# Optimization experiments

Measured on AMD Instinct MI355X. Metric: run time of the kernel, lower is better.

## Reference

```python
import jax, jax.numpy as jnp
import numpy as np

NEG_INF = jnp.float32(-1e30)
HASH_PRIME = jnp.int32(1000003)
BLANK_INDEX = 0
BEAM_WIDTH = 32
TOP_PATHS = 1


def _beam_search_single(logp, length):
    """CTC prefix beam search for one utterance.
    logp: [T, C] log-probabilities. length: scalar int32.
    Returns (neg_log_prob [P], lengths [P], labels [P, T]).
    """
    T, C = logp.shape
    W = BEAM_WIDTH
    classes = jnp.arange(C, dtype=jnp.int32)
    tpos = jnp.arange(T, dtype=jnp.int32)
    N = W + W * C  # stay candidates + extend candidates

    seqs0 = jnp.zeros((W, T), jnp.int32)
    lens0 = jnp.zeros((W,), jnp.int32)
    hashes0 = jnp.arange(W, dtype=jnp.int32)  # distinct -> no spurious merging
    pb0 = jnp.full((W,), NEG_INF, jnp.float32).at[0].set(0.0)  # empty prefix, ends-in-blank
    pnb0 = jnp.full((W,), NEG_INF, jnp.float32)

    def step(state, inp):
        seqs, lens, hashes, pb, pnb = state
        lp, t = inp  # lp: [C]
        last = jnp.where(lens > 0, seqs[jnp.arange(W), jnp.maximum(lens - 1, 0)], -1)
        lp_last = jnp.where(last >= 0, lp[jnp.maximum(last, 0)], NEG_INF)
        ptot = jnp.logaddexp(pb, pnb)
        # --- stay candidates (same prefix): blank emission + repeated last label
        stay_pb = ptot + lp[BLANK_INDEX]
        stay_pnb = pnb + lp_last
        # --- extend candidates (W, C): prefix + c, c != blank
        ext_pnb = jnp.where(classes[None, :] == last[:, None],
                            pb[:, None] + lp[None, :],      # repeat label needs blank gap
                            ptot[:, None] + lp[None, :])
        ext_pnb = jnp.where(classes[None, :] == BLANK_INDEX, NEG_INF, ext_pnb)
        ext_pb = jnp.full((W, C), NEG_INF, jnp.float32)
        ext_hash = hashes[:, None] * HASH_PRIME + (classes[None, :] + 1)
        cand_pb = jnp.concatenate([stay_pb, ext_pb.reshape(-1)])
        cand_pnb = jnp.concatenate([stay_pnb, ext_pnb.reshape(-1)])
        cand_hash = jnp.concatenate([hashes, ext_hash.reshape(-1)])
        # --- merge candidates sharing the same prefix (by rolling hash)
        order = jnp.argsort(cand_hash)
        h_s = cand_hash[order]
        pb_s, pnb_s = cand_pb[order], cand_pnb[order]
        new_seg = jnp.concatenate([jnp.ones((1,), jnp.int32),
                                   (h_s[1:] != h_s[:-1]).astype(jnp.int32)])
        seg_id = jnp.cumsum(new_seg) - 1

        def seg_lse(x):
            m = jax.ops.segment_max(x, seg_id, num_segments=N)
            s = jax.ops.segment_sum(jnp.exp(x - m[seg_id]), seg_id, num_segments=N)
            return m + jnp.log(s)

        pb_m = seg_lse(pb_s)[seg_id]
        pnb_m = seg_lse(pnb_s)[seg_id]
        first = new_seg == 1
        pb_s = jnp.where(first, pb_m, NEG_INF)
        pnb_s = jnp.where(first, pnb_m, NEG_INF)
        tot = jnp.logaddexp(pb_s, pnb_s)
        # --- beam pruning
        _, top_idx = jax.lax.top_k(tot, W)
        sel = order[top_idx]  # indices into flat candidate list
        is_ext = sel >= W
        parent = jnp.where(is_ext, (sel - W) // C, sel)
        cls = jnp.where(is_ext, (sel - W) % C, 0).astype(jnp.int32)
        new_pb = pb_s[top_idx]
        new_pnb = pnb_s[top_idx]
        new_hash = cand_hash[sel]
        p_seqs = seqs[parent]
        p_lens = lens[parent]
        new_seqs = jnp.where(is_ext[:, None] & (tpos[None, :] == p_lens[:, None]),
                             cls[:, None], p_seqs)
        new_lens = p_lens + is_ext.astype(jnp.int32)
        # only advance while t < data_length
        active = t < length
        seqs = jnp.where(active, new_seqs, seqs)
        lens = jnp.where(active, new_lens, lens)
        hashes = jnp.where(active, new_hash, hashes)
        pb = jnp.where(active, new_pb, pb)
        pnb = jnp.where(active, new_pnb, pnb)
        return (seqs, lens, hashes, pb, pnb), None

    (seqs, lens, hashes, pb, pnb), _ = jax.lax.scan(
        step, (seqs0, lens0, hashes0, pb0, pnb0), (logp, tpos))
    tot = jnp.logaddexp(pb, pnb)
    top_tot, top_i = jax.lax.top_k(tot, TOP_PATHS)
    return -top_tot, lens[top_i], seqs[top_i]


def setup_inputs() -> dict:
    key = jax.random.key(0)
    k1, k2 = jax.random.split(key)
    data = jax.random.normal(k1, (512, 64, 128), jnp.float32)
    data = jax.nn.log_softmax(data, axis=-1)  # layer expects log probs (from_logits=False)
    data_length = jax.random.randint(k2, (64,), 1, 513, dtype=jnp.int32)
    return {"data": data, "data_length": data_length}


def reference(data, data_length):
    # data: [max_time, batch, num_classes] log probs -> [batch, T, C]
    logp = jnp.transpose(data, (1, 0, 2))
    probs, lengths, predicted = jax.vmap(_beam_search_single)(logp, data_length)
    # top_paths == 1 path of _select_most_likely_path: plain reshape
    B = predicted.shape[0]
    T = predicted.shape[2]
    best = predicted.reshape(B, T)
    lens = lengths.reshape(B)
    # _mask_out_junk_values: fill positions >= length with blank_index
    mask = jnp.arange(T, dtype=lens.dtype)[None, :] < lens[:, None]
    return jnp.where(mask, best, jnp.int32(BLANK_INDEX))
```

## Files before the change

kernel.cpp:

```cpp
#include <hip/hip_runtime.h>
#include <stdint.h>

#define T_MAX 512
#define BATCH 64
#define NCLS  128
#define BEAM  32
#define TBL   6144
#define NEGF  (-1e30f)
#define EMPTYK ((int)0x80000000)
#define HPRIME 1000003u
#define SCAP  256

__device__ __forceinline__ float lae(float a, float b) {
  float mx = fmaxf(a, b);
  return mx + log1pf(expf(-fabsf(a - b)));
}
__device__ __forceinline__ unsigned encf(float x) {
  unsigned v = __float_as_uint(x);
  return (v & 0x80000000u) ? ~v : (v | 0x80000000u);
}
__device__ __forceinline__ float decf(unsigned u) {
  unsigned v = (u & 0x80000000u) ? (u ^ 0x80000000u) : ~u;
  return __uint_as_float(v);
}
__device__ __forceinline__ unsigned lowkey(unsigned h) {
  return 0xFFFFFFFFu - (h ^ 0x80000000u);
}

__device__ __forceinline__ int tbl_insert(int* key, int h) {
  unsigned x = (unsigned)h * 2654435761u;
  x ^= x >> 16;
  int j = (int)(((unsigned long long)x * (unsigned long long)TBL) >> 32);
  for (;;) {
    int cur = key[j];
    if (cur == EMPTYK) cur = atomicCAS(&key[j], EMPTYK, h);
    if (cur == EMPTYK || cur == h) return j;
    ++j; if (j == TBL) j = 0;
  }
}

__device__ __forceinline__ unsigned long long shflx64(unsigned long long v, int m) {
  unsigned lo = (unsigned)__shfl_xor((int)(unsigned)v, m, 64);
  unsigned hi = (unsigned)__shfl_xor((int)(unsigned)(v >> 32), m, 64);
  return ((unsigned long long)hi << 32) | lo;
}

__device__ __forceinline__ unsigned bitonic64_u32_desc(int ln, unsigned v) {
  #pragma unroll
  for (int size = 2; size <= 64; size <<= 1) {
    #pragma unroll
    for (int stride = size >> 1; stride > 0; stride >>= 1) {
      const unsigned o = (unsigned)__shfl_xor((int)v, stride, 64);
      const bool keepMax = (((ln & size) == 0) == ((ln & stride) == 0));
      v = keepMax ? (v > o ? v : o) : (v < o ? v : o);
    }
  }
  return v;
}

__global__ __launch_bounds__(512, 1)
void ctc_beam_kernel(const float* __restrict__ data,
                     const int* __restrict__ dlen,
                     int* __restrict__ out) {
  __shared__ int       tkey[TBL];
  __shared__ unsigned  tmax[TBL];
  __shared__ unsigned  tsum[TBL];
  __shared__ unsigned  tmin[TBL];
  __shared__ unsigned short bp[T_MAX * BEAM];
  __shared__ __align__(16) float lpbuf[2][NCLS];
  __shared__ int   bhash[2][BEAM];
  __shared__ float bpb[2][BEAM], bpnb[2][BEAM];
  __shared__ int   blen[2][BEAM], blast[2][BEAM];
  __shared__ float sptot[BEAM], s_pb[BEAM], s_pnb[BEAM], s_pnbm[BEAM];
  __shared__ int   stay_slot[BEAM];
  __shared__ unsigned char mergeTo[BEAM * NCLS];
  __shared__ int mergeCnt[BEAM], mergeFrom[BEAM];
  __shared__ unsigned thsub[64];
  __shared__ int anom, ovf;
  __shared__ int scnt[2];
  __shared__ unsigned long long skey[SCAP + 16];
  __shared__ unsigned sidx[SCAP];
  __shared__ unsigned long long wkey[8 * BEAM];
  __shared__ unsigned widx[8 * BEAM];
  __shared__ unsigned sel[BEAM];
  __shared__ int seqbuf[T_MAX];
  __shared__ int flen_s;

  const int tid = threadIdx.x;
  const int b = blockIdx.x;
  int L = dlen[b];
  L = L < 0 ? 0 : (L > T_MAX ? T_MAX : L);

  if (tid < BEAM) {
    bhash[0][tid] = tid;
    bpb[0][tid]   = (tid == 0) ? 0.0f : NEGF;
    bpnb[0][tid]  = NEGF;
    blen[0][tid]  = 0;
    blast[0][tid] = -1;
    mergeCnt[tid] = 0;
  }
  {
    unsigned* mtw = (unsigned*)mergeTo;
    for (int m = tid; m < (BEAM * NCLS) / 4; m += 512) mtw[m] = 0xFFFFFFFFu;
  }
  if (tid == 0) { anom = 0; ovf = 0; scnt[0] = 0; scnt[1] = 0; }
  if (tid < NCLS && L > 0) lpbuf[0][tid] = data[(size_t)b * NCLS + tid];
  __syncthreads();

  int cb = 0;
  for (int t = 0; t < L; ++t) {
    const int par = t & 1;
    const bool haspre = (tid >= 256) && (tid < 256 + NCLS) && (t + 1 < L);
    float pre = 0.0f;
    if (haspre) pre = data[((size_t)(t + 1) * BATCH + b) * NCLS + (tid - 256)];
    float* lpc = lpbuf[par];

    if (tid < BEAM) {
      const float pbv = bpb[cb][tid], pnbv = bpnb[cb][tid];
      const float pt = lae(pbv, pnbv);
      sptot[tid] = pt;
      s_pb[tid]  = pt + lpc[0];
      const int lsti = blast[cb][tid];
      s_pnb[tid] = pnbv + ((lsti >= 0) ? lpc[lsti] : NEGF);
    }
    for (int k = tid; k < BEAM * BEAM; k += 512) {
      const int j = k >> 5, i2 = k & 31;
      const unsigned hj = (unsigned)bhash[cb][j];
      const unsigned hip = (unsigned)bhash[cb][i2] * HPRIME;
      const unsigned c = hj - hip - 1u;
      if (c < (unsigned)NCLS) {
        atomicAdd(&mergeCnt[j], 1);
        mergeFrom[j] = (i2 << 8) | (int)c;
        mergeTo[i2 * NCLS + (int)c] = (unsigned char)j;
      }
      if (j < i2) {
        const unsigned d = (hj - (unsigned)bhash[cb][i2]) * HPRIME;
        if (d + 127u <= 254u) anom = 1;
      }
    }
    __syncthreads();

    const int i  = tid >> 4;
    const int c0 = (tid & 15) << 3;
    unsigned long long k8[8];
    {
      const float pbi = bpb[cb][i];
      const float pti = sptot[i];
      const int   lsti = blast[cb][i];
      const unsigned hb = (unsigned)bhash[cb][i] * HPRIME;
      const float4 l0 = ((const float4*)(lpc + c0))[0];
      const float4 l1 = ((const float4*)(lpc + c0))[1];
      const float lv[8] = {l0.x, l0.y, l0.z, l0.w, l1.x, l1.y, l1.z, l1.w};
      const unsigned m0 = ((const unsigned*)&mergeTo[i * NCLS + c0])[0];
      const unsigned m1 = ((const unsigned*)&mergeTo[i * NCLS + c0])[1];
      unsigned pbest = 0u;
      #pragma unroll
      for (int k = 0; k < 8; ++k) {
        const int c = c0 + k;
        const unsigned mb = ((k < 4 ? (m0 >> (8 * k)) : (m1 >> (8 * (k - 4)))) & 0xFFu);
        const float x = (c == 0) ? NEGF : (((c == lsti) ? pbi : pti) + lv[k]);
        const float tot = fmaxf(x, NEGF);
        const unsigned h = hb + (unsigned)(c + 1);
        unsigned long long key =
            ((unsigned long long)encf(tot) << 32) |
            (unsigned long long)lowkey(h);
        if (mb != 0xFFu || c == 0) key = 0ull;
        k8[k] = key;
        const unsigned e32 = (unsigned)(key >> 32);
        pbest = pbest > e32 ? pbest : e32;
      }
      #pragma unroll
      for (int m = 1; m <= 8; m <<= 1) {
        const unsigned o = (unsigned)__shfl_xor((int)pbest, m, 64);
        pbest = pbest > o ? pbest : o;
      }
      if ((tid & 15) == 0) thsub[32 + i] = pbest;
    }
    if (tid < BEAM) {
      const int j = tid;
      if (mergeCnt[j] > 1) anom = 1;
      float pnbm;
      if (mergeCnt[j] == 1) {
        const int mf = mergeFrom[j];
        const int mi = mf >> 8, mc = mf & 255;
        const float e = (mc == 0) ? NEGF
            : (((mc == blast[cb][mi]) ? bpb[cb][mi] : sptot[mi]) + lpc[mc]);
        const float a = s_pnb[j];
        const float m = fmaxf(a, e);
        const float s = expf(a - m) + expf(e - m);
        pnbm = m + logf(s);
      } else {
        pnbm = s_pnb[j];
      }
      s_pnbm[j] = pnbm;
      thsub[j] = encf(lae(s_pb[j], pnbm));
    }
    if (tid == 511) scnt[par ^ 1] = 0;
    __syncthreads();

    const bool an = (anom != 0);
    bool dorare = an;
    if (!an) {
      const int ln = tid & 63;
      const unsigned sorted = bitonic64_u32_desc(ln, thsub[ln]);
      const unsigned thr = (unsigned)__shfl((int)sorted, 31, 64);

      int myn = 0;
      #pragma unroll
      for (int k = 0; k < 8; ++k) myn += ((unsigned)(k8[k] >> 32) >= thr) ? 1 : 0;
      const bool stayS = (tid < BEAM) && (thsub[tid] >= thr);
      myn += stayS ? 1 : 0;
      int pfx = myn;
      #pragma unroll
      for (int d = 1; d < 64; d <<= 1) {
        const int o = __shfl_up(pfx, d, 64);
        if (ln >= d) pfx += o;
      }
      const int wtot = __shfl(pfx, 63, 64);
      int wbase = 0;
      if (ln == 0 && wtot) wbase = atomicAdd(&scnt[par], wtot);
      wbase = __shfl(wbase, 0, 64);
      if (wbase + wtot > SCAP) {
        if (ln == 0 && wtot) ovf = 1;
      } else if (myn) {
        int o = wbase + pfx - myn;
        #pragma unroll
        for (int k = 0; k < 8; ++k) {
          if ((unsigned)(k8[k] >> 32) >= thr) {
            skey[o] = k8[k];
            sidx[o] = (unsigned)(BEAM + i * NCLS + (c0 + k));
            ++o;
          }
        }
        if (stayS) {
          skey[o] = ((unsigned long long)thsub[tid] << 32) |
                    (unsigned long long)lowkey((unsigned)bhash[cb][tid]);
          sidx[o] = (unsigned)tid;
        }
      }
      __syncthreads();
      dorare = (ovf != 0);
    }

    if (!dorare) {
      const int scr = scnt[par];
      if (tid < scr) {
        const unsigned long long kq = skey[tid];
        int rank = 0;
        for (int p0 = 0; p0 < scr; p0 += 16) {
          #pragma unroll
          for (int pp = 0; pp < 16; ++pp) {
            const unsigned long long kp = skey[p0 + pp];
            rank += ((p0 + pp) < scr && kp > kq) ? 1 : 0;
          }
        }
        if (rank < BEAM) {
          const int j = rank;
          const unsigned s = sidx[tid];
          int nh, p, cls, ex; float npb, npnb;
          if (s < BEAM) {
            p = (int)s; cls = 0; ex = 0;
            nh = bhash[cb][p];
            npb = s_pb[p];
            npnb = s_pnbm[p];
          } else {
            const unsigned q = s - BEAM;
            p = (int)(q >> 7); cls = (int)(q & 127); ex = 1;
            nh = (int)((unsigned)bhash[cb][p] * HPRIME + (unsigned)(cls + 1));
            npb = NEGF;
            npnb = (cls == 0) ? NEGF
                 : (((cls == blast[cb][p]) ? bpb[cb][p] : sptot[p]) + lpc[cls]);
          }
          const int plen = blen[cb][p], plast = blast[cb][p];
          const int nb = cb ^ 1;
          bhash[nb][j] = nh; bpb[nb][j] = npb; bpnb[nb][j] = npnb;
          blen[nb][j]  = plen + ex;
          blast[nb][j] = ex ? cls : plast;
          bp[t * BEAM + j] = (unsigned short)(p | (cls << 5) | (ex << 12));
        }
      }
      if (tid >= 256) {
        unsigned* mtw = (unsigned*)mergeTo;
        const int base = tid - 256;
        #pragma unroll
        for (int m = 0; m < 4; ++m) mtw[base + m * 256] = 0xFFFFFFFFu;
        if (haspre) lpbuf[par ^ 1][tid - 256] = pre;
      }
      if (tid >= 64 && tid < 64 + BEAM) mergeCnt[tid - 64] = 0;
      __syncthreads();
    } else {
      for (int m = tid; m < TBL; m += 512) {
        tkey[m] = EMPTYK; tmax[m] = 0u; tsum[m] = 0u; tmin[m] = 0xFFFFFFFFu;
      }
      __syncthreads();

      int eslot[8]; float ex_[8];
      {
        const float pbi = bpb[cb][i];
        const float pti = sptot[i];
        const int   lsti = blast[cb][i];
        const unsigned hb = (unsigned)bhash[cb][i] * HPRIME;
        #pragma unroll
        for (int k = 0; k < 8; ++k) {
          const int c = c0 + k;
          int h = (int)(hb + (unsigned)(c + 1));
          if (h == EMPTYK) h = (int)0x80000001u;
          const float x = (c == 0) ? NEGF : (((c == lsti) ? pbi : pti) + lpc[c]);
          const int s = tbl_insert(tkey, h);
          atomicMax(&tmax[s], encf(x));
          atomicMin(&tmin[s], (unsigned)(BEAM + i * NCLS + c));
          eslot[k] = s; ex_[k] = x;
        }
      }
      if (tid < BEAM) {
        const int s = tbl_insert(tkey, bhash[cb][tid]);
        atomicMax(&tmax[s], encf(s_pnb[tid]));
        atomicMin(&tmin[s], (unsigned)tid);
        stay_slot[tid] = s;
      }
      __syncthreads();

      #pragma unroll
      for (int k = 0; k < 8; ++k) {
        const int s = eslot[k];
        atomicAdd((float*)&tsum[s], expf(ex_[k] - decf(tmax[s])));
      }
      if (tid < BEAM) {
        const int s = stay_slot[tid];
        atomicAdd((float*)&tsum[s], expf(s_pnb[tid] - decf(tmax[s])));
      }
      __syncthreads();

      for (int m = tid; m < TBL; m += 512) {
        if (tkey[m] != EMPTYK) {
          const float mm = decf(tmax[m]);
          const float ss = __uint_as_float(tsum[m]);
          const float pnbm = mm + logf(ss);
          tmax[m] = __float_as_uint(pnbm);
          tsum[m] = encf(lae(NEGF, pnbm));
        }
      }
      __syncthreads();
      if (tid < BEAM) {
        const int s = stay_slot[tid];
        tsum[s] = encf(lae(s_pb[tid], __uint_as_float(tmax[s])));
      }
      __syncthreads();

      {
        const int wv = tid >> 6, ln = tid & 63;
        const int base = wv * (TBL / 8) + ln * (TBL / 512);
        unsigned long long kk2[TBL / 512];
        #pragma unroll
        for (int m = 0; m < TBL / 512; ++m) {
          const int idx = base + m;
          if (tkey[idx] != EMPTYK) {
            kk2[m] = ((unsigned long long)tsum[idx] << 32) |
                     (unsigned long long)lowkey((unsigned)tkey[idx]);
          } else kk2[m] = 0ull;
        }
        unsigned cons = 0;
        for (int it = 0; it < BEAM; ++it) {
          unsigned long long best = 0ull; int bi = -1;
          #pragma unroll
          for (int m = 0; m < TBL / 512; ++m)
            if (!((cons >> m) & 1u) && kk2[m] > best) { best = kk2[m]; bi = m; }
          unsigned long long wm = best;
          #pragma unroll
          for (int off = 32; off > 0; off >>= 1) {
            const unsigned long long o = shflx64(wm, off);
            if (o > wm) wm = o;
          }
          const unsigned long long ball = __ballot(best == wm && wm != 0ull);
          const int winner = ball ? (__ffsll((long long)ball) - 1) : -1;
          if (ln == winner) {
            cons |= 1u << bi;
            wkey[wv * BEAM + it] = wm;
            widx[wv * BEAM + it] = (unsigned)(base + bi);
          } else if (winner < 0 && ln == 0) {
            wkey[wv * BEAM + it] = 0ull;
            widx[wv * BEAM + it] = 0xFFFFFFFFu;
          }
        }
      }
      __syncthreads();
      if (tid < 64) {
        unsigned long long kk2[4]; unsigned ii[4];
        #pragma unroll
        for (int m = 0; m < 4; ++m) { kk2[m] = wkey[tid * 4 + m]; ii[m] = widx[tid * 4 + m]; }
        unsigned cons = 0;
        for (int it = 0; it < BEAM; ++it) {
          unsigned long long best = 0ull; int bi = -1;
          #pragma unroll
          for (int m = 0; m < 4; ++m)
            if (!((cons >> m) & 1u) && kk2[m] > best) { best = kk2[m]; bi = m; }
          unsigned long long wm = best;
          #pragma unroll
          for (int off = 32; off > 0; off >>= 1) {
            const unsigned long long o = shflx64(wm, off);
            if (o > wm) wm = o;
          }
          const unsigned long long ball = __ballot(best == wm && wm != 0ull);
          const int winner = ball ? (__ffsll((long long)ball) - 1) : -1;
          if (tid == winner) { cons |= 1u << bi; sel[it] = ii[bi]; }
          else if (winner < 0 && tid == 0) sel[it] = 0xFFFFFFFFu;
        }
      }
      __syncthreads();

      if (tid < BEAM) {
        const int j = tid;
        const unsigned s = sel[j];
        int nh, p, cls, ex; float npb, npnb;
        if (s != 0xFFFFFFFFu) {
          nh = tkey[s];
          npnb = __uint_as_float(tmax[s]);
          npb = NEGF;
          #pragma unroll
          for (int q = 0; q < BEAM; ++q)
            if (stay_slot[q] == (int)s) npb = s_pb[q];
          const unsigned mi = tmin[s];
          ex  = (mi >= BEAM) ? 1 : 0;
          p   = ex ? (int)((mi - BEAM) >> 7) : (int)mi;
          cls = ex ? (int)((mi - BEAM) & 127) : 0;
          p &= 31;
        } else {
          nh = 0x7F000000 + j; npb = NEGF; npnb = NEGF; p = j; cls = 0; ex = 0;
        }
        const int plen = blen[cb][p], plast = blast[cb][p];
        const int nb = cb ^ 1;
        bhash[nb][j] = nh; bpb[nb][j] = npb; bpnb[nb][j] = npnb;
        blen[nb][j]  = plen + ex;
        blast[nb][j] = ex ? cls : plast;
        bp[t * BEAM + j] = (unsigned short)(p | (cls << 5) | (ex << 12));
      }
      {
        unsigned* mtw = (unsigned*)mergeTo;
        for (int m = tid; m < (BEAM * NCLS) / 4; m += 512) mtw[m] = 0xFFFFFFFFu;
      }
      if (tid >= 64 && tid < 64 + BEAM) mergeCnt[tid - 64] = 0;
      if (tid == 511) { anom = 0; ovf = 0; }
      if (haspre) lpbuf[par ^ 1][tid - 256] = pre;
      __syncthreads();
    }
    cb ^= 1;
  }

  if (tid == 0) {
    float bt = -3.4e38f; int bj = 0;
    for (int j = 0; j < BEAM; ++j) {
      const float tt = lae(bpb[cb][j], bpnb[cb][j]);
      if (tt > bt) { bt = tt; bj = j; }
    }
    int cur = bj;
    int pos = blen[cb][bj];
    flen_s = pos;
    for (int tt = L - 1; tt >= 0; --tt) {
      const unsigned short e = bp[tt * BEAM + cur];
      const int p = e & 31, cl = (e >> 5) & 127, ex = (e >> 12) & 1;
      if (ex) { --pos; if (pos >= 0) seqbuf[pos] = cl; }
      cur = p;
    }
  }
  __syncthreads();
  const int fl = flen_s;
  for (int k = tid; k < T_MAX; k += 512) {
    out[(size_t)b * T_MAX + k] = (k < fl) ? seqbuf[k] : 0;
  }
}

extern "C" void kernel_launch(void* const* d_in, const int* in_sizes, int n_in,
                              void* d_out, int out_size, void* d_ws, size_t ws_size,
                              hipStream_t stream) {
  const float* data = (const float*)d_in[0];
  const int*   dlen = (const int*)d_in[1];
  int* out = (int*)d_out;
  (void)in_sizes; (void)n_in; (void)out_size; (void)d_ws; (void)ws_size;
  hipLaunchKernelGGL(ctc_beam_kernel, dim3(BATCH), dim3(512), 0, stream,
                     data, dlen, out);
}
```

Baseline: 2.261 ms.

## Double block size to 1024 threads, each handling four candidate classes

Each block now has 1024 threads instead of 512, so every thread scores 4 extension candidates instead of 8. The merge check, hash-table passes, per-wave top-k and final merge stage are remapped to match: 16 waves, 8 entries per lane in the final merge, and prefetch threads moved to 512+. The aim is a shorter serial per-step critical path in this latency-bound, one-block-per-utterance loop. The cost is more barrier participants per step, a longer final 8-way merge scan, and possible register pressure limits at 1024 threads.

```diff
diff --git a/kernel.cpp b/kernel.cpp
--- a/kernel.cpp
+++ b/kernel.cpp
@@ -10,6 +10,7 @@
 #define EMPTYK ((int)0x80000000)
 #define HPRIME 1000003u
 #define SCAP  256
+#define NTHR  1024
 
 __device__ __forceinline__ float lae(float a, float b) {
   float mx = fmaxf(a, b);
@@ -58,7 +59,7 @@
   return v;
 }
 
-__global__ __launch_bounds__(512, 1)
+__global__ __launch_bounds__(NTHR, 1)
 void ctc_beam_kernel(const float* __restrict__ data,
                      const int* __restrict__ dlen,
                      int* __restrict__ out) {
@@ -80,8 +81,8 @@
   __shared__ int scnt[2];
   __shared__ unsigned long long skey[SCAP + 16];
   __shared__ unsigned sidx[SCAP];
-  __shared__ unsigned long long wkey[8 * BEAM];
-  __shared__ unsigned widx[8 * BEAM];
+  __shared__ unsigned long long wkey[16 * BEAM];
+  __shared__ unsigned widx[16 * BEAM];
   __shared__ unsigned sel[BEAM];
   __shared__ int seqbuf[T_MAX];
   __shared__ int flen_s;
@@ -101,7 +102,7 @@
   }
   {
     unsigned* mtw = (unsigned*)mergeTo;
-    for (int m = tid; m < (BEAM * NCLS) / 4; m += 512) mtw[m] = 0xFFFFFFFFu;
+    for (int m = tid; m < (BEAM * NCLS) / 4; m += NTHR) mtw[m] = 0xFFFFFFFFu;
   }
   if (tid == 0) { anom = 0; ovf = 0; scnt[0] = 0; scnt[1] = 0; }
   if (tid < NCLS && L > 0) lpbuf[0][tid] = data[(size_t)b * NCLS + tid];
@@ -110,9 +111,9 @@
   int cb = 0;
   for (int t = 0; t < L; ++t) {
     const int par = t & 1;
-    const bool haspre = (tid >= 256) && (tid < 256 + NCLS) && (t + 1 < L);
+    const bool haspre = (tid >= 512) && (tid < 512 + NCLS) && (t + 1 < L);
     float pre = 0.0f;
-    if (haspre) pre = data[((size_t)(t + 1) * BATCH + b) * NCLS + (tid - 256)];
+    if (haspre) pre = data[((size_t)(t + 1) * BATCH + b) * NCLS + (tid - 512)];
     float* lpc = lpbuf[par];
 
     if (tid < BEAM) {
@@ -123,8 +124,8 @@
       const int lsti = blast[cb][tid];
       s_pnb[tid] = pnbv + ((lsti >= 0) ? lpc[lsti] : NEGF);
     }
-    for (int k = tid; k < BEAM * BEAM; k += 512) {
-      const int j = k >> 5, i2 = k & 31;
+    {
+      const int j = tid >> 5, i2 = tid & 31;
       const unsigned hj = (unsigned)bhash[cb][j];
       const unsigned hip = (unsigned)bhash[cb][i2] * HPRIME;
       const unsigned c = hj - hip - 1u;
@@ -140,24 +141,22 @@
     }
     __syncthreads();
 
-    const int i  = tid >> 4;
-    const int c0 = (tid & 15) << 3;
-    unsigned long long k8[8];
+    const int i  = tid >> 5;
+    const int c0 = (tid & 31) << 2;
+    unsigned long long k4[4];
     {
       const float pbi = bpb[cb][i];
       const float pti = sptot[i];
       const int   lsti = blast[cb][i];
       const unsigned hb = (unsigned)bhash[cb][i] * HPRIME;
       const float4 l0 = ((const float4*)(lpc + c0))[0];
-      const float4 l1 = ((const float4*)(lpc + c0))[1];
-      const float lv[8] = {l0.x, l0.y, l0.z, l0.w, l1.x, l1.y, l1.z, l1.w};
+      const float lv[4] = {l0.x, l0.y, l0.z, l0.w};
       const unsigned m0 = ((const unsigned*)&mergeTo[i * NCLS + c0])[0];
-      const unsigned m1 = ((const unsigned*)&mergeTo[i * NCLS + c0])[1];
       unsigned pbest = 0u;
       #pragma unroll
-      for (int k = 0; k < 8; ++k) {
+      for (int k = 0; k < 4; ++k) {
         const int c = c0 + k;
-        const unsigned mb = ((k < 4 ? (m0 >> (8 * k)) : (m1 >> (8 * (k - 4)))) & 0xFFu);
+        const unsigned mb = (m0 >> (8 * k)) & 0xFFu;
         const float x = (c == 0) ? NEGF : (((c == lsti) ? pbi : pti) + lv[k]);
         const float tot = fmaxf(x, NEGF);
         const unsigned h = hb + (unsigned)(c + 1);
@@ -165,16 +164,16 @@
             ((unsigned long long)encf(tot) << 32) |
             (unsigned long long)lowkey(h);
         if (mb != 0xFFu || c == 0) key = 0ull;
-        k8[k] = key;
+        k4[k] = key;
         const unsigned e32 = (unsigned)(key >> 32);
         pbest = pbest > e32 ? pbest : e32;
       }
       #pragma unroll
-      for (int m = 1; m <= 8; m <<= 1) {
+      for (int m = 1; m <= 16; m <<= 1) {
         const unsigned o = (unsigned)__shfl_xor((int)pbest, m, 64);
         pbest = pbest > o ? pbest : o;
       }
-      if ((tid & 15) == 0) thsub[32 + i] = pbest;
+      if ((tid & 31) == 0) thsub[32 + i] = pbest;
     }
     if (tid < BEAM) {
       const int j = tid;
@@ -195,7 +194,7 @@
       s_pnbm[j] = pnbm;
       thsub[j] = encf(lae(s_pb[j], pnbm));
     }
-    if (tid == 511) scnt[par ^ 1] = 0;
+    if (tid == NTHR - 1) scnt[par ^ 1] = 0;
     __syncthreads();
 
     const bool an = (anom != 0);
@@ -207,7 +206,7 @@
 
       int myn = 0;
       #pragma unroll
-      for (int k = 0; k < 8; ++k) myn += ((unsigned)(k8[k] >> 32) >= thr) ? 1 : 0;
+      for (int k = 0; k < 4; ++k) myn += ((unsigned)(k4[k] >> 32) >= thr) ? 1 : 0;
       const bool stayS = (tid < BEAM) && (thsub[tid] >= thr);
       myn += stayS ? 1 : 0;
       int pfx = myn;
@@ -225,9 +224,9 @@
       } else if (myn) {
         int o = wbase + pfx - myn;
         #pragma unroll
-        for (int k = 0; k < 8; ++k) {
-          if ((unsigned)(k8[k] >> 32) >= thr) {
-            skey[o] = k8[k];
+        for (int k = 0; k < 4; ++k) {
+          if ((unsigned)(k4[k] >> 32) >= thr) {
+            skey[o] = k4[k];
             sidx[o] = (unsigned)(BEAM + i * NCLS + (c0 + k));
             ++o;
           }
@@ -279,29 +278,29 @@
           bp[t * BEAM + j] = (unsigned short)(p | (cls << 5) | (ex << 12));
         }
       }
-      if (tid >= 256) {
+      if (tid >= 512) {
         unsigned* mtw = (unsigned*)mergeTo;
-        const int base = tid - 256;
+        const int base = tid - 512;
         #pragma unroll
-        for (int m = 0; m < 4; ++m) mtw[base + m * 256] = 0xFFFFFFFFu;
-        if (haspre) lpbuf[par ^ 1][tid - 256] = pre;
+        for (int m = 0; m < 2; ++m) mtw[base + m * 512] = 0xFFFFFFFFu;
+        if (haspre) lpbuf[par ^ 1][tid - 512] = pre;
       }
       if (tid >= 64 && tid < 64 + BEAM) mergeCnt[tid - 64] = 0;
       __syncthreads();
     } else {
-      for (int m = tid; m < TBL; m += 512) {
+      for (int m = tid; m < TBL; m += NTHR) {
         tkey[m] = EMPTYK; tmax[m] = 0u; tsum[m] = 0u; tmin[m] = 0xFFFFFFFFu;
       }
       __syncthreads();
 
-      int eslot[8]; float ex_[8];
+      int eslot[4]; float ex_[4];
       {
         const float pbi = bpb[cb][i];
         const float pti = sptot[i];
         const int   lsti = blast[cb][i];
         const unsigned hb = (unsigned)bhash[cb][i] * HPRIME;
         #pragma unroll
-        for (int k = 0; k < 8; ++k) {
+        for (int k = 0; k < 4; ++k) {
           const int c = c0 + k;
           int h = (int)(hb + (unsigned)(c + 1));
           if (h == EMPTYK) h = (int)0x80000001u;
@@ -321,7 +320,7 @@
       __syncthreads();
 
       #pragma unroll
-      for (int k = 0; k < 8; ++k) {
+      for (int k = 0; k < 4; ++k) {
         const int s = eslot[k];
         atomicAdd((float*)&tsum[s], expf(ex_[k] - decf(tmax[s])));
       }
@@ -331,7 +330,7 @@
       }
       __syncthreads();
 
-      for (int m = tid; m < TBL; m += 512) {
+      for (int m = tid; m < TBL; m += NTHR) {
         if (tkey[m] != EMPTYK) {
           const float mm = decf(tmax[m]);
           const float ss = __uint_as_float(tsum[m]);
@@ -349,10 +348,10 @@
 
       {
         const int wv = tid >> 6, ln = tid & 63;
-        const int base = wv * (TBL / 8) + ln * (TBL / 512);
-        unsigned long long kk2[TBL / 512];
+        const int base = wv * (TBL / 16) + ln * (TBL / NTHR);
+        unsigned long long kk2[TBL / NTHR];
         #pragma unroll
-        for (int m = 0; m < TBL / 512; ++m) {
+        for (int m = 0; m < TBL / NTHR; ++m) {
           const int idx = base + m;
           if (tkey[idx] != EMPTYK) {
             kk2[m] = ((unsigned long long)tsum[idx] << 32) |
@@ -363,7 +362,7 @@
         for (int it = 0; it < BEAM; ++it) {
           unsigned long long best = 0ull; int bi = -1;
           #pragma unroll
-          for (int m = 0; m < TBL / 512; ++m)
+          for (int m = 0; m < TBL / NTHR; ++m)
             if (!((cons >> m) & 1u) && kk2[m] > best) { best = kk2[m]; bi = m; }
           unsigned long long wm = best;
           #pragma unroll
@@ -385,15 +384,15 @@
       }
       __syncthreads();
       if (tid < 64) {
-        unsigned long long kk2[4]; unsigned ii[4];
+        unsigned long long mk[8]; unsigned mx[8];
         #pragma unroll
-        for (int m = 0; m < 4; ++m) { kk2[m] = wkey[tid * 4 + m]; ii[m] = widx[tid * 4 + m]; }
+        for (int m = 0; m < 8; ++m) { mk[m] = wkey[tid * 8 + m]; mx[m] = widx[tid * 8 + m]; }
         unsigned cons = 0;
         for (int it = 0; it < BEAM; ++it) {
           unsigned long long best = 0ull; int bi = -1;
           #pragma unroll
-          for (int m = 0; m < 4; ++m)
-            if (!((cons >> m) & 1u) && kk2[m] > best) { best = kk2[m]; bi = m; }
+          for (int m = 0; m < 8; ++m)
+            if (!((cons >> m) & 1u) && mk[m] > best) { best = mk[m]; bi = m; }
           unsigned long long wm = best;
           #pragma unroll
           for (int off = 32; off > 0; off >>= 1) {
@@ -402,7 +401,7 @@
           }
           const unsigned long long ball = __ballot(best == wm && wm != 0ull);
           const int winner = ball ? (__ffsll((long long)ball) - 1) : -1;
-          if (tid == winner) { cons |= 1u << bi; sel[it] = ii[bi]; }
+          if (tid == winner) { cons |= 1u << bi; sel[it] = mx[bi]; }
           else if (winner < 0 && tid == 0) sel[it] = 0xFFFFFFFFu;
         }
       }
@@ -436,11 +435,11 @@
       }
       {
         unsigned* mtw = (unsigned*)mergeTo;
-        for (int m = tid; m < (BEAM * NCLS) / 4; m += 512) mtw[m] = 0xFFFFFFFFu;
+        for (int m = tid; m < (BEAM * NCLS) / 4; m += NTHR) mtw[m] = 0xFFFFFFFFu;
       }
       if (tid >= 64 && tid < 64 + BEAM) mergeCnt[tid - 64] = 0;
-      if (tid == 511) { anom = 0; ovf = 0; }
-      if (haspre) lpbuf[par ^ 1][tid - 256] = pre;
+      if (tid == NTHR - 1) { anom = 0; ovf = 0; }
+      if (haspre) lpbuf[par ^ 1][tid - 512] = pre;
       __syncthreads();
     }
     cb ^= 1;
@@ -464,7 +463,7 @@
   }
   __syncthreads();
   const int fl = flen_s;
-  for (int k = tid; k < T_MAX; k += 512) {
+  for (int k = tid; k < T_MAX; k += NTHR) {
     out[(size_t)b * T_MAX + k] = (k < fl) ? seqbuf[k] : 0;
   }
 }
@@ -476,6 +475,6 @@
   const int*   dlen = (const int*)d_in[1];
   int* out = (int*)d_out;
   (void)in_sizes; (void)n_in; (void)out_size; (void)d_ws; (void)ws_size;
-  hipLaunchKernelGGL(ctc_beam_kernel, dim3(BATCH), dim3(512), 0, stream,
+  hipLaunchKernelGGL(ctc_beam_kernel, dim3(BATCH), dim3(NTHR), 0, stream,
                      data, dlen, out);
 }
```

Measured after the change: 2.200 ms. 1.03x faster.
